# Kernel tuning notes

Hardware: AMD Instinct MI355X
Metric: run time of the kernel (lower is better)

## Reference

```python
import jax, jax.numpy as jnp
import numpy as np

B = 8
C = 256
N40, N20, N10 = 1600, 400, 100
N = N40 + N20 + N10  # 2100 pixel nodes (40x40 + 20x20 + 10x10)

def _grid_edges(h, w, off):
    # 8-neighborhood 'contextual' edges within one scale's grid
    idx = np.arange(h * w).reshape(h, w)
    srcs, dsts = [], []
    for di in (-1, 0, 1):
        for dj in (-1, 0, 1):
            if di == 0 and dj == 0:
                continue
            s = idx[max(0, -di):h - max(0, di), max(0, -dj):w - max(0, dj)]
            d = idx[max(0, di):h - max(0, -di), max(0, dj):w - max(0, -dj)]
            srcs.append(off + s.ravel())
            dsts.append(off + d.ravel())
    return srcs, dsts

def _hier_edges(ph, pw, poff, coff):
    # bidirected parent <-> 4-children 'hierarchical' edges between scales
    i, j = np.meshgrid(np.arange(ph), np.arange(pw), indexing='ij')
    parent = (poff + i * pw + j).ravel()
    srcs, dsts = [], []
    cw = 2 * pw
    for di in (0, 1):
        for dj in (0, 1):
            child = (coff + (2 * i + di) * cw + (2 * j + dj)).ravel()
            srcs += [parent, child]
            dsts += [child, parent]
    return srcs, dsts

def build_edges():
    loop = [np.arange(N)]  # dgl.add_self_loop on both etypes
    cs, cd = [], []
    for (h, w, off) in ((40, 40, 0), (20, 20, N40), (10, 10, N40 + N20)):
        s, d = _grid_edges(h, w, off)
        cs += s; cd += d
    ctx_src = np.concatenate(cs + loop); ctx_dst = np.concatenate(cd + loop)
    hs, hd = [], []
    s, d = _hier_edges(20, 20, N40, 0); hs += s; hd += d
    s, d = _hier_edges(10, 10, N40 + N20, N40); hs += s; hd += d
    hier_src = np.concatenate(hs + loop); hier_dst = np.concatenate(hd + loop)
    return (jnp.asarray(ctx_src, jnp.int32), jnp.asarray(ctx_dst, jnp.int32),
            jnp.asarray(hier_src, jnp.int32), jnp.asarray(hier_dst, jnp.int32))

def _bn_relu(x, g, b, m, v):
    # inference-mode BatchNorm2d + ReLU
    scale = g * jax.lax.rsqrt(v + 1e-5)
    return jax.nn.relu(x * scale[:, None, None] + (b - m * scale)[:, None, None])

def _conv1x1(x, w, b):
    return jnp.einsum('bchw,oc->bohw', x, w) + b[:, None, None]

def _avgpool2(x):
    b, c, h, w = x.shape
    return x.reshape(b, c, h // 2, 2, w // 2, 2).mean(axis=(3, 5))

def _up2(x):
    return jnp.repeat(jnp.repeat(x, 2, axis=2), 2, axis=3)

def _gnn(h, src, dst, deg_inv, w, b):
    # gather -> scatter-add -> mean over in-neighbors (incl. self loop) -> linear -> ReLU
    agg = jnp.zeros_like(h).at[:, dst].add(h[:, src]) * deg_inv[None, :, None]
    return jax.nn.relu(jnp.einsum('bnc,cd->bnd', agg, w) + b)

def _convT2x2(x, wt, b):
    # stride-2 2x2 transposed conv; wt: [Cin, Cout, 2, 2] (torch layout)
    bsz, cin, h, w = x.shape
    y = jnp.einsum('bchw,cokl->bohkwl', x, wt)
    return y.reshape(bsz, wt.shape[1], 2 * h, 2 * w) + b[:, None, None]

def setup_inputs():
    key = jax.random.key(0)
    ks = iter(jax.random.split(key, 64))
    def rn(shape, scale=0.02):
        return jax.random.normal(next(ks), shape, jnp.float32) * scale
    inp = {}
    inp['feat0'] = rn((B, 256, 160, 160), 1.0)
    inp['feat1'] = rn((B, 512, 80, 80), 1.0)
    inp['feat2'] = rn((B, 1024, 40, 40), 1.0)
    inp['feat3'] = rn((B, 2048, 20, 20), 1.0)
    for i, cin in ((1, 512), (2, 1024), (3, 2048)):
        inp['dw%d' % i] = rn((256, cin))
        inp['db%d' % i] = jnp.zeros((256,), jnp.float32)
        inp['g%d' % i] = jnp.ones((256,), jnp.float32)
        inp['b%d' % i] = jnp.zeros((256,), jnp.float32)
        inp['m%d' % i] = jnp.zeros((256,), jnp.float32)
        inp['v%d' % i] = jnp.ones((256,), jnp.float32)
    for i in range(1, 7):
        inp['gW%d' % i] = rn((256, 256))
        inp['gb%d' % i] = jnp.zeros((256,), jnp.float32)
    for i, cout in ((1, 512), (2, 1024), (3, 2048)):
        inp['tW%d' % i] = rn((256, cout, 2, 2))
        inp['tb%d' % i] = jnp.zeros((cout,), jnp.float32)
    ctx_src, ctx_dst, hier_src, hier_dst = build_edges()
    inp['ctx_src'] = ctx_src; inp['ctx_dst'] = ctx_dst
    inp['hier_src'] = hier_src; inp['hier_dst'] = hier_dst
    return inp

def reference(feat0, feat1, feat2, feat3,
              dw1, db1, g1, b1, m1, v1,
              dw2, db2, g2, b2, m2, v2,
              dw3, db3, g3, b3, m3, v3,
              gW1, gb1, gW2, gb2, gW3, gb3, gW4, gb4, gW5, gb5, gW6, gb6,
              tW1, tb1, tW2, tb2, tW3, tb3,
              ctx_src, ctx_dst, hier_src, hier_dst):
    f40 = _avgpool2(_bn_relu(_conv1x1(feat1, dw1, db1), g1, b1, m1, v1))  # [B,256,40,40]
    f20 = _avgpool2(_bn_relu(_conv1x1(feat2, dw2, db2), g2, b2, m2, v2))  # [B,256,20,20]
    f10 = _avgpool2(_bn_relu(_conv1x1(feat3, dw3, db3), g3, b3, m3, v3))  # [B,256,10,10]
    bsz = f40.shape[0]
    # cnn_gnn: flatten all three scales into [B, 2100, 256] node features (batched
    # version of the original per-sample python loop; graph is identical per sample)
    h = jnp.concatenate([
        f40.reshape(bsz, C, N40).transpose(0, 2, 1),
        f20.reshape(bsz, C, N20).transpose(0, 2, 1),
        f10.reshape(bsz, C, N10).transpose(0, 2, 1)], axis=1)
    dic = 1.0 / jnp.zeros((N,), h.dtype).at[ctx_dst].add(1.0)
    dih = 1.0 / jnp.zeros((N,), h.dtype).at[hier_dst].add(1.0)
    # context1, context2, hierarch1, hierarch2, context4, context5
    h = _gnn(h, ctx_src, ctx_dst, dic, gW1, gb1)
    h = _gnn(h, ctx_src, ctx_dst, dic, gW2, gb2)
    h = _gnn(h, hier_src, hier_dst, dih, gW3, gb3)
    h = _gnn(h, hier_src, hier_dst, dih, gW4, gb4)
    h = _gnn(h, ctx_src, ctx_dst, dic, gW5, gb5)
    h = _gnn(h, ctx_src, ctx_dst, dic, gW6, gb6)
    # gnn_cnn: split back to NCHW maps
    f40g = h[:, :N40].transpose(0, 2, 1).reshape(bsz, C, 40, 40)
    f20g = h[:, N40:N40 + N20].transpose(0, 2, 1).reshape(bsz, C, 20, 20)
    f10g = h[:, N40 + N20:].transpose(0, 2, 1).reshape(bsz, C, 10, 10)
    f10_ref = f10 + f10g
    f20_ref = f20 + f20g + _up2(f10g)
    f40_ref = f40 + f40g + _up2(f20g)
    out1 = _convT2x2(f40_ref, tW1, tb1) + feat1
    out2 = _convT2x2(f20_ref, tW2, tb2) + feat2
    out3 = _convT2x2(f10_ref, tW3, tb3) + feat3
    return (feat0, out1, out2, out3)
```

## Files before the change

### kernel.cpp

```cpp
#include <hip/hip_runtime.h>
#include <cstdint>

#define NODES 2100

typedef __attribute__((ext_vector_type(8))) __bf16 bf16x8;
typedef __attribute__((ext_vector_type(4))) float f32x4;
typedef __attribute__((ext_vector_type(8))) unsigned short u16x8;

__device__ inline float bf2f(unsigned short s) { return __uint_as_float(((unsigned)s) << 16); }
__device__ inline unsigned short f2bf(float f) {
    unsigned u = __float_as_uint(f);
    u += 0x7fff + ((u >> 16) & 1);
    return (unsigned short)(u >> 16);
}
__device__ inline void gload16(const unsigned short* g, void* lds) {
    __builtin_amdgcn_global_load_lds(
        (const __attribute__((address_space(1))) void*)g,
        (__attribute__((address_space(3))) void*)lds, 16, 0, 0);
}

__device__ inline size_t pk(int row, int k, int nK) {
    return ((size_t)((row >> 4) * nK + (k >> 5)) << 9)
         + ((((k >> 3) & 3) << 4) + (row & 15)) * 8 + (k & 7);
}

struct PrepArgs {
    const float *dw0, *dw1, *dw2;
    const float *gw0, *gw1, *gw2, *gw3, *gw4, *gw5;
    const float *tw0, *tw1, *tw2;
    const float *g0, *g1, *g2, *b0, *b1, *b2, *m0, *m1, *m2, *v0, *v1, *v2, *db0, *db1, *db2;
    unsigned short *dwb, *gWTb, *tWTb;
    float *scshb;
};

__device__ inline void transpose32p(const float* __restrict__ in, unsigned short* __restrict__ outT,
                                    int Ccols, int c0, int r0)
{
    __shared__ float T[32][33];
    const int tx = threadIdx.x & 31, ty = threadIdx.x >> 5;
#pragma unroll
    for (int i = 0; i < 4; ++i)
        T[ty + i * 8][tx] = in[(size_t)(r0 + ty + i * 8) * Ccols + c0 + tx];
    __syncthreads();
#pragma unroll
    for (int i = 0; i < 4; ++i) {
        int Rrow = c0 + ty + i * 8;
        int k    = r0 + tx;
        outT[pk(Rrow, k, 8)] = f2bf(T[tx][ty + i * 8]);
    }
}

__global__ __launch_bounds__(256)
void mega_prep(PrepArgs a)
{
    int bid = blockIdx.x;
    const int t = threadIdx.x;
    if (bid < 448) {
        int idx = (bid * 256 + t) * 8;
        const float* src; unsigned short* dst; int loc, K;
        if (idx < 131072)      { src = a.dw0; dst = a.dwb;          loc = idx;          K = 512; }
        else if (idx < 393216) { src = a.dw1; dst = a.dwb + 131072; loc = idx - 131072; K = 1024; }
        else                   { src = a.dw2; dst = a.dwb + 393216; loc = idx - 393216; K = 2048; }
        int row = loc / K, k = loc - row * K;
        float4 x = *(const float4*)(src + loc);
        float4 y = *(const float4*)(src + loc + 4);
        u16x8 r;
        r[0] = f2bf(x.x); r[1] = f2bf(x.y); r[2] = f2bf(x.z); r[3] = f2bf(x.w);
        r[4] = f2bf(y.x); r[5] = f2bf(y.y); r[6] = f2bf(y.z); r[7] = f2bf(y.w);
        *(u16x8*)(dst + pk(row, k, K >> 5)) = r;
    } else if (bid < 832) {
        int gid = bid - 448;
        int l = gid >> 6, sb = gid & 63;
        const float* gw[6] = {a.gw0, a.gw1, a.gw2, a.gw3, a.gw4, a.gw5};
        transpose32p(gw[l], a.gWTb + (size_t)l * 65536, 256, (sb & 7) << 5, (sb >> 3) << 5);
    } else if (bid < 4416) {
        int gid = bid - 832;
        const float* tw; unsigned short* dst; int ncx, loc;
        if (gid < 512)       { tw = a.tw0; dst = a.tWTb;           ncx = 64;  loc = gid; }
        else if (gid < 1536) { tw = a.tw1; dst = a.tWTb + 524288;  ncx = 128; loc = gid - 512; }
        else                 { tw = a.tw2; dst = a.tWTb + 1572864; ncx = 256; loc = gid - 1536; }
        int cx = loc % ncx, ry = loc / ncx;
        transpose32p(tw, dst, ncx * 32, cx << 5, ry << 5);
    } else {
        const float* g[3]  = {a.g0, a.g1, a.g2};
        const float* b[3]  = {a.b0, a.b1, a.b2};
        const float* m[3]  = {a.m0, a.m1, a.m2};
        const float* v[3]  = {a.v0, a.v1, a.v2};
        const float* db[3] = {a.db0, a.db1, a.db2};
        for (int s = 0; s < 3; ++s) {
            float sc = g[s][t] * rsqrtf(v[s][t] + 1e-5f);
            a.scshb[s * 512 + t] = sc;
            a.scshb[s * 512 + 256 + t] = (db[s][t] - m[s][t]) * sc + b[s][t];
        }
    }
}

struct ConvArgs {
    const float* feat[3];
    const unsigned short* dwb[3];
    const float* scsh[3];
    unsigned short* h0out;
};

__global__ __launch_bounds__(256)
void conv_fused(ConvArgs ca)
{
    __shared__ __align__(16) unsigned short As[2][64 * 64];
    int bx = blockIdx.x;
    int s, mt;
    if (bx < 800)       { s = 0; mt = bx; }
    else if (bx < 1000) { s = 1; mt = bx - 800; }
    else                { s = 2; mt = bx - 1000; }
    const int Kc[3]  = {512, 1024, 2048};
    const int Wc[3]  = {80, 40, 20};
    const int PPc[3] = {1600, 400, 100};
    const int nfc[3] = {0, 1600, 2000};
    const int K = Kc[s], W = Wc[s], W2 = W >> 1, HW = W * W, PP = PPc[s], noff = nfc[s];
    const int nK = K >> 5;
    const float* feat = ca.feat[s];
    const unsigned short* dw = ca.dwb[s];
    const float* scsh = ca.scsh[s];

    const int t = threadIdx.x, lane = t & 63, w = t >> 6;
    const int sx = (lane & 7) << 4;

    const int ml = t & 63;
    const int kw = t >> 6;
    const int graw = mt * 64 + ml;
    const int b = graw / HW;
    const int rem = graw - b * HW;
    const int pooled = rem >> 2, sub = rem & 3;
    const int pi = pooled / W2, pj = pooled - pi * W2;
    const int i = pi * 2 + (sub >> 1), j = pj * 2 + (sub & 1);
    const float* src = feat + (size_t)b * K * HW + (size_t)i * W + j;
    const int sxm = (ml & 7) << 3;

    f32x4 acc[4][4];
#pragma unroll
    for (int fr = 0; fr < 4; ++fr)
#pragma unroll
        for (int fc = 0; fc < 4; ++fc) acc[fr][fc] = (f32x4){0.f, 0.f, 0.f, 0.f};

    float vC[16], vN[16];
#pragma unroll
    for (int it = 0; it < 16; ++it)
        vC[it] = src[(size_t)(it * 4 + kw) * HW];

    int buf = 0;
    for (int k0 = 0; k0 < K; k0 += 64) {
        unsigned short* Ab = As[buf];
#pragma unroll
        for (int it = 0; it < 16; ++it) {
            int k_l = it * 4 + kw;
            Ab[(ml << 6) + (k_l ^ sxm)] = f2bf(vC[it]);
        }
        __syncthreads();
        if (k0 + 64 < K) {
#pragma unroll
            for (int it = 0; it < 16; ++it)
                vN[it] = src[(size_t)(k0 + 64 + it * 4 + kw) * HW];
        }
#pragma unroll
        for (int kk = 0; kk < 2; ++kk) {
            bf16x8 a[4], bb[4];
#pragma unroll
            for (int f = 0; f < 4; ++f) {
                int pa = ((((f * 16 + (lane & 15)) << 7) + kk * 64 + ((lane >> 4) << 4)) ^ sx);
                a[f] = *(const bf16x8*)((const char*)Ab + pa);
                bb[f] = *(const bf16x8*)(dw + ((size_t)(((w << 2) + f) * nK + (k0 >> 5) + kk) << 9) + (lane << 3));
            }
#pragma unroll
            for (int fr = 0; fr < 4; ++fr)
#pragma unroll
                for (int fc = 0; fc < 4; ++fc)
                    acc[fr][fc] = __builtin_amdgcn_mfma_f32_16x16x32_bf16(a[fr], bb[fc], acc[fr][fc], 0, 0, 0);
        }
#pragma unroll
        for (int it = 0; it < 16; ++it) vC[it] = vN[it];
        buf ^= 1;
    }

#pragma unroll
    for (int fc = 0; fc < 4; ++fc) {
        const int o = w * 64 + fc * 16 + (lane & 15);
        const float sc = scsh[o], sh = scsh[256 + o];
#pragma unroll
        for (int fr = 0; fr < 4; ++fr) {
            const int mrow = mt * 64 + fr * 16 + (lane >> 4) * 4;
            const int q = mrow >> 2;
            const int bi = q / PP;
            const int node = noff + (q - bi * PP);
            float sum = 0.f;
#pragma unroll
            for (int r = 0; r < 4; ++r)
                sum += fmaxf(acc[fr][fc][r] * sc + sh, 0.f);
            ca.h0out[((size_t)(bi * NODES + node)) * 256 + o] = f2bf(sum * 0.25f);
        }
    }
}

__global__ __launch_bounds__(256)
void gnn_fused(const unsigned short* __restrict__ h, const unsigned short* __restrict__ BT,
               const float* __restrict__ bias, unsigned short* __restrict__ out, int hier)
{
    __shared__ __align__(16) unsigned short As[2][32 * 64];
    const int t = threadIdx.x, lane = t & 63, w = t >> 6;
    const int r0 = blockIdx.x << 5;
    const int myrow = t >> 3, q = t & 7;
    const int grow = r0 + myrow;
    const int b = grow / NODES;
    const int n = grow - b * NODES;

    int gw, off;
    if (n < 1600)      { gw = 40; off = 0; }
    else if (n < 2000) { gw = 20; off = 1600; }
    else               { gw = 10; off = 2000; }
    const int li = (n - off) / gw;
    const int lj = (n - off) - li * gw;
    int nbr[9]; int cnt = 0;
    if (!hier) {
#pragma unroll
        for (int di = -1; di <= 1; ++di)
#pragma unroll
            for (int dj = -1; dj <= 1; ++dj) {
                int ii = li + di, jj = lj + dj;
                if (ii >= 0 && ii < gw && jj >= 0 && jj < gw) nbr[cnt++] = off + ii * gw + jj;
            }
    } else {
        nbr[cnt++] = n;
        if (off == 0) {
            nbr[cnt++] = 1600 + (li >> 1) * 20 + (lj >> 1);
        } else if (off == 1600) {
            nbr[cnt++] = 2000 + (li >> 1) * 10 + (lj >> 1);
#pragma unroll
            for (int di = 0; di < 2; ++di)
#pragma unroll
                for (int dj = 0; dj < 2; ++dj)
                    nbr[cnt++] = ((li << 1) + di) * 40 + ((lj << 1) + dj);
        } else {
#pragma unroll
            for (int di = 0; di < 2; ++di)
#pragma unroll
                for (int dj = 0; dj < 2; ++dj)
                    nbr[cnt++] = 1600 + ((li << 1) + di) * 20 + ((lj << 1) + dj);
        }
    }
    int nboff[9];
#pragma unroll
    for (int e = 0; e < 9; ++e)
        nboff[e] = (b * NODES + nbr[e < cnt ? e : 0]) * 256 + q * 8;
    const float inv = 1.0f / (float)cnt;
    const int sx = (lane & 7) << 4;
    const int awr = (myrow << 6) + ((q ^ (myrow & 7)) << 3);

    f32x4 acc[2][4];
#pragma unroll
    for (int fr = 0; fr < 2; ++fr)
#pragma unroll
        for (int fc = 0; fc < 4; ++fc) acc[fr][fc] = (f32x4){0.f, 0.f, 0.f, 0.f};

    u16x8 pre[9];
#pragma unroll
    for (int e = 0; e < 9; ++e) pre[e] = *(const u16x8*)(h + nboff[e]);

    int buf = 0;
    for (int k0 = 0; k0 < 256; k0 += 64) {
        float sacc[8] = {0, 0, 0, 0, 0, 0, 0, 0};
#pragma unroll
        for (int e = 0; e < 9; ++e) {
            if (e < cnt) {
#pragma unroll
                for (int jj = 0; jj < 8; ++jj) sacc[jj] += bf2f(pre[e][jj]);
            }
        }
        u16x8 o0;
#pragma unroll
        for (int jj = 0; jj < 8; ++jj) o0[jj] = f2bf(sacc[jj] * inv);
        *(u16x8*)&As[buf][awr] = o0;
        __syncthreads();

        const int k0n = (k0 + 64) & 255;
#pragma unroll
        for (int e = 0; e < 9; ++e) pre[e] = *(const u16x8*)(h + nboff[e] + k0n);

        const unsigned short* Ab = As[buf];
#pragma unroll
        for (int kk = 0; kk < 2; ++kk) {
            bf16x8 a[2], bb[4];
#pragma unroll
            for (int f = 0; f < 2; ++f) {
                int pa = ((((f * 16 + (lane & 15)) << 7) + kk * 64 + ((lane >> 4) << 4)) ^ sx);
                a[f] = *(const bf16x8*)((const char*)Ab + pa);
            }
#pragma unroll
            for (int f = 0; f < 4; ++f)
                bb[f] = *(const bf16x8*)(BT + ((size_t)(((w << 2) + f) * 8 + (k0 >> 5) + kk) << 9) + (lane << 3));
#pragma unroll
            for (int fr = 0; fr < 2; ++fr)
#pragma unroll
                for (int fc = 0; fc < 4; ++fc)
                    acc[fr][fc] = __builtin_amdgcn_mfma_f32_16x16x32_bf16(a[fr], bb[fc], acc[fr][fc], 0, 0, 0);
        }
        buf ^= 1;
    }

#pragma unroll
    for (int fc = 0; fc < 4; ++fc) {
        const int d = w * 64 + fc * 16 + (lane & 15);
        const float bv = bias[d];
#pragma unroll
        for (int fr = 0; fr < 2; ++fr) {
            int rb = r0 + fr * 16 + (lane >> 4) * 4;
#pragma unroll
            for (int r = 0; r < 4; ++r)
                out[(size_t)(rb + r) * 256 + d] = f2bf(fmaxf(acc[fr][fc][r] + bv, 0.f));
        }
    }
}

__global__ __launch_bounds__(256)
void a_build(const unsigned short* __restrict__ h0, const unsigned short* __restrict__ h6,
             unsigned short* __restrict__ Ao)
{
    int bx = blockIdx.x;
    int P, H2, noff, pbase, pw, haspar, rows; size_t aoff;
    if (bx < 1600)      { P = 1600; H2 = 40; noff = 0;    pbase = 1600; pw = 20; haspar = 1; aoff = 0;               rows = 12800; }
    else if (bx < 2000) { P = 400;  H2 = 20; noff = 1600; pbase = 2000; pw = 10; haspar = 1; aoff = 12800ULL * 256; rows = 3200; bx -= 1600; }
    else                { P = 100;  H2 = 10; noff = 2000; pbase = 0;    pw = 0;  haspar = 0; aoff = 16000ULL * 256; rows = 800;  bx -= 2000; }
    const int gid = bx * 256 + threadIdx.x;
    const int m = gid >> 5, c0 = (gid & 31) << 3;
    unsigned short* dst = Ao + aoff + (((size_t)((m >> 4) * 8 + (c0 >> 5))) << 9)
                        + ((((c0 >> 3) & 3) << 4) + (m & 15)) * 8;
    if (m >= rows) {
        u16x8 z = (u16x8){0, 0, 0, 0, 0, 0, 0, 0};
        *(u16x8*)dst = z;
        return;
    }
    const int b = m / P, pix = m - b * P;
    const size_t src = ((size_t)(b * NODES + noff + pix)) * 256 + c0;
    u16x8 x0 = *(const u16x8*)(h0 + src);
    u16x8 x6 = *(const u16x8*)(h6 + src);
    float v[8];
#pragma unroll
    for (int e = 0; e < 8; ++e) v[e] = bf2f(x0[e]) + bf2f(x6[e]);
    if (haspar) {
        int ii = pix / H2, jj = pix - ii * H2;
        size_t sp = ((size_t)(b * NODES + pbase + (ii >> 1) * pw + (jj >> 1))) * 256 + c0;
        u16x8 xp = *(const u16x8*)(h6 + sp);
#pragma unroll
        for (int e = 0; e < 8; ++e) v[e] += bf2f(xp[e]);
    }
    u16x8 r;
#pragma unroll
    for (int e = 0; e < 8; ++e) r[e] = f2bf(v[e]);
    *(u16x8*)dst = r;
}

struct ConvtArgs {
    const unsigned short* WT[3];
    const unsigned short* Apix[3];
    const float* tb[3];
    const float* feat[3];
    float* out[3];
    const float4* cps; float4* cpd;
};

__global__ __launch_bounds__(256)
void convt_fused(ConvtArgs ct)
{
    __shared__ __align__(16) unsigned short Sb[2][16 * 512];
    int bx = blockIdx.x;
    if (bx < 1024) {
        const int base = bx * 256 + threadIdx.x;
        const int stride = 1024 * 256;
        const float4* s = ct.cps;
        float4* d = ct.cpd;
        for (int j = 0; j < 50; j += 5) {
            float4 v0 = s[base + (size_t)(j + 0) * stride];
            float4 v1 = s[base + (size_t)(j + 1) * stride];
            float4 v2 = s[base + (size_t)(j + 2) * stride];
            float4 v3 = s[base + (size_t)(j + 3) * stride];
            float4 v4 = s[base + (size_t)(j + 4) * stride];
            d[base + (size_t)(j + 0) * stride] = v0;
            d[base + (size_t)(j + 1) * stride] = v1;
            d[base + (size_t)(j + 2) * stride] = v2;
            d[base + (size_t)(j + 3) * stride] = v3;
            d[base + (size_t)(j + 4) * stride] = v4;
        }
        return;
    }
    bx -= 1024;
    int s, px, my;
    if (bx < 6400) {
        s = 0;
        int L = (bx & 7) * 800 + (bx >> 3);
        px = L >> 5; my = L & 31;
    } else if (bx < 9600) {
        s = 1; bx -= 6400;
        int L = (bx & 7) * 400 + (bx >> 3);
        px = L >> 6; my = L & 63;
    } else {
        s = 2; bx -= 9600;
        int L = (bx & 7) * 208 + (bx >> 3);
        my = L / 13; px = L - my * 13;
    }
    const int Pc[3]  = {1600, 400, 100};
    const int H2c[3] = {40, 20, 10};
    const int Cc[3]  = {512, 1024, 2048};
    const int Mc[3]  = {12800, 3200, 800};
    const int P = Pc[s], H2 = H2c[s], Cout = Cc[s], Mpix = Mc[s];
    const int m0 = my << 6, n0 = px << 6;
    const int m0u = my << 2, n0u = px << 2;
    const unsigned short* WT = ct.WT[s];
    const unsigned short* Apix = ct.Apix[s];

    const int t = threadIdx.x, lane = t & 63, w = t >> 6;
    const int wr = w >> 1, wc = w & 1;

    auto STAGE = [&](int c, int bsel) {
#pragma unroll
        for (int ul = 0; ul < 4; ++ul) {
            int u = (w << 2) + ul;
            const unsigned short* src;
            if (w < 2) {
                int ru = u >> 1, ch = u & 1;
                src = WT + ((size_t)((m0u + ru) * 8 + c * 2 + ch) << 9) + (lane << 3);
            } else {
                int v = u - 8;
                int ru = v >> 1, ch = v & 1;
                src = Apix + ((size_t)((n0u + ru) * 8 + c * 2 + ch) << 9) + (lane << 3);
            }
            gload16(src, (char*)&Sb[bsel][0] + u * 1024 + lane * 16);
        }
    };

    f32x4 acc[2][2];
#pragma unroll
    for (int fr = 0; fr < 2; ++fr)
#pragma unroll
        for (int fc = 0; fc < 2; ++fc) acc[fr][fc] = (f32x4){0.f, 0.f, 0.f, 0.f};

    STAGE(0, 0);
    __syncthreads();
#pragma unroll
    for (int c = 0; c < 4; ++c) {
        if (c < 3) STAGE(c + 1, (c + 1) & 1);
        const unsigned short* B = &Sb[c & 1][0];
#pragma unroll
        for (int kk = 0; kk < 2; ++kk) {
            bf16x8 a[2], bb[2];
#pragma unroll
            for (int f = 0; f < 2; ++f) {
                a[f]  = *(const bf16x8*)(B + (((wr * 2 + f) * 2 + kk) << 9) + (lane << 3));
                bb[f] = *(const bf16x8*)(B + ((8 + (wc * 2 + f) * 2 + kk) << 9) + (lane << 3));
            }
#pragma unroll
            for (int fr = 0; fr < 2; ++fr)
#pragma unroll
                for (int fc = 0; fc < 2; ++fc)
                    acc[fr][fc] = __builtin_amdgcn_mfma_f32_16x16x32_bf16(a[fr], bb[fc], acc[fr][fc], 0, 0, 0);
        }
        __syncthreads();
    }

    const int H = H2 * 2;
    const float* feat = ct.feat[s];
    float* out = ct.out[s];
#pragma unroll
    for (int fc = 0; fc < 2; ++fc) {
        const int p_g = n0 + wc * 32 + fc * 16 + (lane & 15);
        if (p_g < Mpix) {
            const int b = p_g / P, pix = p_g - b * P;
            const int ii = pix / H2, jj = pix - ii * H2;
#pragma unroll
            for (int fr = 0; fr < 2; ++fr) {
                const int rb = m0 + wr * 32 + fr * 16 + (lane >> 4) * 4;
                const int o = rb >> 2;
                const float tbo = ct.tb[s][o];
                size_t base = (((size_t)(b * Cout + o)) * H + 2 * ii) * H + 2 * jj;
                float2 f0 = *(const float2*)&feat[base];
                float2 r0v; r0v.x = acc[fr][fc][0] + tbo + f0.x; r0v.y = acc[fr][fc][1] + tbo + f0.y;
                *(float2*)&out[base] = r0v;
                float2 f1 = *(const float2*)&feat[base + H];
                float2 r1v; r1v.x = acc[fr][fc][2] + tbo + f1.x; r1v.y = acc[fr][fc][3] + tbo + f1.y;
                *(float2*)&out[base + H] = r1v;
            }
        }
    }
}

extern "C" void kernel_launch(void* const* d_in, const int* in_sizes, int n_in,
                              void* d_out, int out_size, void* d_ws, size_t ws_size,
                              hipStream_t stream)
{
    const float* feats[3] = { (const float*)d_in[1], (const float*)d_in[2], (const float*)d_in[3] };
    const float* gb[6];
    for (int l = 0; l < 6; ++l) gb[l] = (const float*)d_in[23 + 2 * l];
    const float* tb[3] = { (const float*)d_in[35], (const float*)d_in[37], (const float*)d_in[39] };

    size_t off = 0;
    auto alloc = [&](size_t bytes) { size_t r = off; off = (off + bytes + 511) & ~(size_t)511; return r; };
    unsigned short* h0b  = (unsigned short*)((char*)d_ws + alloc(16800ULL * 256 * 2));
    unsigned short* hA   = (unsigned short*)((char*)d_ws + alloc(16800ULL * 256 * 2));
    unsigned short* hB   = (unsigned short*)((char*)d_ws + alloc(16800ULL * 256 * 2));
    unsigned short* dwb  = (unsigned short*)((char*)d_ws + alloc(917504ULL * 2));
    unsigned short* gWTb = (unsigned short*)((char*)d_ws + alloc(6ULL * 65536 * 2));
    unsigned short* tWTb = (unsigned short*)((char*)d_ws + alloc(3670016ULL * 2));
    float*          scshb= (float*)((char*)d_ws + alloc(3ULL * 512 * 4));
    unsigned short* Aconvt = (unsigned short*)((char*)d_ws + off);

    PrepArgs pa;
    pa.dw0 = (const float*)d_in[4];  pa.dw1 = (const float*)d_in[10]; pa.dw2 = (const float*)d_in[16];
    pa.gw0 = (const float*)d_in[22]; pa.gw1 = (const float*)d_in[24]; pa.gw2 = (const float*)d_in[26];
    pa.gw3 = (const float*)d_in[28]; pa.gw4 = (const float*)d_in[30]; pa.gw5 = (const float*)d_in[32];
    pa.tw0 = (const float*)d_in[34]; pa.tw1 = (const float*)d_in[36]; pa.tw2 = (const float*)d_in[38];
    pa.g0 = (const float*)d_in[6];  pa.g1 = (const float*)d_in[12]; pa.g2 = (const float*)d_in[18];
    pa.b0 = (const float*)d_in[7];  pa.b1 = (const float*)d_in[13]; pa.b2 = (const float*)d_in[19];
    pa.m0 = (const float*)d_in[8];  pa.m1 = (const float*)d_in[14]; pa.m2 = (const float*)d_in[20];
    pa.v0 = (const float*)d_in[9];  pa.v1 = (const float*)d_in[15]; pa.v2 = (const float*)d_in[21];
    pa.db0 = (const float*)d_in[5]; pa.db1 = (const float*)d_in[11]; pa.db2 = (const float*)d_in[17];
    pa.dwb = dwb; pa.gWTb = gWTb; pa.tWTb = tWTb; pa.scshb = scshb;
    mega_prep<<<dim3(4417), dim3(256), 0, stream>>>(pa);

    ConvArgs ca;
    ca.feat[0] = feats[0]; ca.feat[1] = feats[1]; ca.feat[2] = feats[2];
    ca.dwb[0] = dwb; ca.dwb[1] = dwb + 131072; ca.dwb[2] = dwb + 393216;
    ca.scsh[0] = scshb; ca.scsh[1] = scshb + 512; ca.scsh[2] = scshb + 1024;
    ca.h0out = h0b;
    conv_fused<<<dim3(1050), dim3(256), 0, stream>>>(ca);

    const int types[6] = {0, 0, 1, 1, 0, 0};
    const unsigned short* hin = h0b;
    unsigned short* houts[6] = {hA, hB, hA, hB, hA, hB};
    for (int l = 0; l < 6; ++l) {
        gnn_fused<<<dim3(525), dim3(256), 0, stream>>>(
            hin, gWTb + (size_t)l * 65536, gb[l], houts[l], types[l]);
        hin = houts[l];
    }
    unsigned short* h6 = hB;

    a_build<<<dim3(2104), dim3(256), 0, stream>>>(h0b, h6, Aconvt);

    ConvtArgs ct;
    ct.WT[0] = tWTb; ct.WT[1] = tWTb + 524288; ct.WT[2] = tWTb + 1572864;
    ct.Apix[0] = Aconvt; ct.Apix[1] = Aconvt + 12800ULL * 256; ct.Apix[2] = Aconvt + 16000ULL * 256;
    ct.tb[0] = tb[0]; ct.tb[1] = tb[1]; ct.tb[2] = tb[2];
    ct.feat[0] = feats[0]; ct.feat[1] = feats[1]; ct.feat[2] = feats[2];
    ct.out[0] = (float*)d_out + 52428800;
    ct.out[1] = (float*)d_out + 52428800 + 26214400;
    ct.out[2] = (float*)d_out + 52428800 + 26214400 + 13107200;
    ct.cps = (const float4*)d_in[0];
    ct.cpd = (float4*)d_out;
    convt_fused<<<dim3(1024 + 11264), dim3(256), 0, stream>>>(ct);
}
```

Measured before the change: 456.2 us.

## Load full K panel into LDS at once in convt and widen copy grid

Replaces the double-buffered four-stage K loop in the transposed-conv GEMM with a single bulk global-to-LDS load of all eight K chunks, followed by one wait and barrier, then eight MFMA steps with no intermediate syncs. LDS per block grows from 32 KB to 64 KB, which may reduce how many blocks fit per CU. The fused feat0 copy portion is split across twice as many blocks, each doing half as many float4 moves.

```diff
diff --git a/kernel.cpp b/kernel.cpp
--- a/kernel.cpp
+++ b/kernel.cpp
@@ -368,14 +368,14 @@
 __global__ __launch_bounds__(256)
 void convt_fused(ConvtArgs ct)
 {
-    __shared__ __align__(16) unsigned short Sb[2][16 * 512];
+    __shared__ __align__(16) unsigned short Sb[64 * 512];
     int bx = blockIdx.x;
-    if (bx < 1024) {
+    if (bx < 2048) {
         const int base = bx * 256 + threadIdx.x;
-        const int stride = 1024 * 256;
+        const int stride = 2048 * 256;
         const float4* s = ct.cps;
         float4* d = ct.cpd;
-        for (int j = 0; j < 50; j += 5) {
+        for (int j = 0; j < 25; j += 5) {
             float4 v0 = s[base + (size_t)(j + 0) * stride];
             float4 v1 = s[base + (size_t)(j + 1) * stride];
             float4 v2 = s[base + (size_t)(j + 2) * stride];
@@ -389,7 +389,7 @@
         }
         return;
     }
-    bx -= 1024;
+    bx -= 2048;
     int s, px, my;
     if (bx < 6400) {
         s = 0;
@@ -417,22 +417,22 @@
     const int t = threadIdx.x, lane = t & 63, w = t >> 6;
     const int wr = w >> 1, wc = w & 1;
 
-    auto STAGE = [&](int c, int bsel) {
-#pragma unroll
-        for (int ul = 0; ul < 4; ++ul) {
-            int u = (w << 2) + ul;
-            const unsigned short* src;
-            if (w < 2) {
-                int ru = u >> 1, ch = u & 1;
-                src = WT + ((size_t)((m0u + ru) * 8 + c * 2 + ch) << 9) + (lane << 3);
-            } else {
-                int v = u - 8;
-                int ru = v >> 1, ch = v & 1;
-                src = Apix + ((size_t)((n0u + ru) * 8 + c * 2 + ch) << 9) + (lane << 3);
-            }
-            gload16(src, (char*)&Sb[bsel][0] + u * 1024 + lane * 16);
-        }
-    };
+#pragma unroll
+    for (int it = 0; it < 16; ++it) {
+        int u = (w << 4) + it;
+        const unsigned short* src;
+        if (u < 32) {
+            int ru = u >> 3, c = u & 7;
+            src = WT + ((size_t)((m0u + ru) * 8 + c) << 9) + (lane << 3);
+        } else {
+            int v = u - 32;
+            int ru = v >> 3, c = v & 7;
+            src = Apix + ((size_t)((n0u + ru) * 8 + c) << 9) + (lane << 3);
+        }
+        gload16(src, (char*)Sb + u * 1024 + lane * 16);
+    }
+    asm volatile("s_waitcnt vmcnt(0)" ::: "memory");
+    __syncthreads();
 
     f32x4 acc[2][2];
 #pragma unroll
@@ -440,27 +440,19 @@
 #pragma unroll
         for (int fc = 0; fc < 2; ++fc) acc[fr][fc] = (f32x4){0.f, 0.f, 0.f, 0.f};
 
-    STAGE(0, 0);
-    __syncthreads();
-#pragma unroll
-    for (int c = 0; c < 4; ++c) {
-        if (c < 3) STAGE(c + 1, (c + 1) & 1);
-        const unsigned short* B = &Sb[c & 1][0];
-#pragma unroll
-        for (int kk = 0; kk < 2; ++kk) {
-            bf16x8 a[2], bb[2];
-#pragma unroll
-            for (int f = 0; f < 2; ++f) {
-                a[f]  = *(const bf16x8*)(B + (((wr * 2 + f) * 2 + kk) << 9) + (lane << 3));
-                bb[f] = *(const bf16x8*)(B + ((8 + (wc * 2 + f) * 2 + kk) << 9) + (lane << 3));
-            }
-#pragma unroll
-            for (int fr = 0; fr < 2; ++fr)
-#pragma unroll
-                for (int fc = 0; fc < 2; ++fc)
-                    acc[fr][fc] = __builtin_amdgcn_mfma_f32_16x16x32_bf16(a[fr], bb[fc], acc[fr][fc], 0, 0, 0);
-        }
-        __syncthreads();
+#pragma unroll
+    for (int c = 0; c < 8; ++c) {
+        bf16x8 a[2], bb[2];
+#pragma unroll
+        for (int f = 0; f < 2; ++f) {
+            a[f]  = *(const bf16x8*)((const char*)Sb + (((wr * 2 + f) * 8 + c) << 10) + (lane << 4));
+            bb[f] = *(const bf16x8*)((const char*)Sb + ((32 + (wc * 2 + f) * 8 + c) << 10) + (lane << 4));
+        }
+#pragma unroll
+        for (int fr = 0; fr < 2; ++fr)
+#pragma unroll
+            for (int fc = 0; fc < 2; ++fc)
+                acc[fr][fc] = __builtin_amdgcn_mfma_f32_16x16x32_bf16(a[fr], bb[fc], acc[fr][fc], 0, 0, 0);
     }
 
     const int H = H2 * 2;
@@ -551,5 +543,5 @@
     ct.out[2] = (float*)d_out + 52428800 + 26214400 + 13107200;
     ct.cps = (const float4*)d_in[0];
     ct.cpd = (float4*)d_out;
-    convt_fused<<<dim3(1024 + 11264), dim3(256), 0, stream>>>(ct);
-}
+    convt_fused<<<dim3(2048 + 11264), dim3(256), 0, stream>>>(ct);
+}
```

Result: slower. 496.6 us (+8.9%).
